# Performance work log

Hardware: AMD Instinct MI355X
Metric: run time of the kernel (lower is better)

## Reference

```python
import jax, jax.numpy as jnp
import numpy as np

NUM_HEADS = 5
TEMP = 0.3
NEG_FILL = -1e-7  # note: NOT -inf; masked entries still contribute ~exp(0) to softmax, faithful to torch code


def setup_inputs() -> dict:
    key = jax.random.key(0)
    k1, k2, k3, k4, k5 = jax.random.split(key, 5)
    B, N, F_IN, F_OUT = 8, 1024, 320, 320
    h = jax.random.normal(k1, (B, N, F_IN), dtype=jnp.float32)
    Wqk = jax.random.normal(k2, (F_IN, 2 * F_IN), dtype=jnp.float32) * (1.0 / np.sqrt(F_IN))
    bqk = jax.random.normal(k3, (2 * F_IN,), dtype=jnp.float32) * 0.01
    weight = jax.random.normal(k4, (F_IN, F_OUT), dtype=jnp.float32) * (1.0 / np.sqrt(F_OUT))
    bias = jax.random.normal(k5, (F_OUT,), dtype=jnp.float32) * 0.01
    return {"h": h, "Wqk": Wqk, "bqk": bqk, "weight": weight, "bias": bias}


def reference(h, Wqk, bqk, weight, bias):
    B, N, F = h.shape
    H = NUM_HEADS
    D = F // H
    # linear -> [b, n, 2F]; einops 'b n (h d qk)' => reshape (b, n, h, d, 2)
    qk = (h @ Wqk + bqk).reshape(B, N, H, D, 2)
    q = jnp.transpose(qk[..., 0], (0, 2, 1, 3))  # b h n d
    k = jnp.transpose(qk[..., 1], (0, 2, 1, 3))  # b h n d
    scale = D ** -0.5
    dots = jnp.einsum('bhqd,bhkd->bhqk', q, k) * scale  # b h n n
    at = dots.sum(axis=1)  # b n n  (sum over heads)
    # sort-based threshold: keep values >= descending-sorted value at index N//6
    thr = jax.lax.top_k(at, N // 6 + 1)[0][..., -1]  # b n
    adj = jnp.where(at < thr[:, :, None], jnp.asarray(NEG_FILL, at.dtype), at)
    attn = jax.nn.softmax(adj / TEMP, axis=2)  # b n n
    out_feature = jnp.einsum('bij,bjd->bid', attn, h)  # values = raw input h
    return out_feature @ weight + bias
```

## Files before the change

### kernel.cpp

```cpp
#include <hip/hip_runtime.h>
#include <hip/hip_fp16.h>


typedef __attribute__((ext_vector_type(8))) _Float16 half8;
typedef __attribute__((ext_vector_type(4))) float f32x4;

__device__ __forceinline__ void stage_tile(const __half* g, __half* lds,
                                           int nrow16, int ld, int wave, int lane) {
    const int r = lane >> 2;
    const int c = ((lane & 3) ^ ((lane >> 3) & 3)) * 8;
    for (int i = wave; i < nrow16; i += 4) {
        const __half* src = g + (long)(i * 16 + r) * ld + c;
        __builtin_amdgcn_global_load_lds(
            (const __attribute__((address_space(1))) unsigned int*)src,
            (__attribute__((address_space(3))) unsigned int*)(lds + i * 512),
            16, 0, 0);
    }
}

template <int EPI>
__device__ __forceinline__ void gemm_body(
    const __half* __restrict__ A, const __half* __restrict__ B,
    void* __restrict__ C, void* __restrict__ C2, const float* __restrict__ bias,
    int lda, int ldb, int ldc, int bx, int by, __half* smem)
{
    constexpr int BUF = 16384;
    const int tid  = threadIdx.x;
    const int lane = tid & 63;
    const int wave = tid >> 6;
    const int wm   = wave >> 1;
    const int wn   = wave & 1;

    const __half* Ab = A + (long)by * 128 * lda;
    const __half* Bb = B + (long)bx * 128 * ldb;

    f32x4 acc[4][4];
    #pragma unroll
    for (int i = 0; i < 4; ++i)
        #pragma unroll
        for (int j = 0; j < 4; ++j) acc[i][j] = (f32x4){0.f, 0.f, 0.f, 0.f};

    const int lrow = lane & 15;
    const int quad = lane >> 4;
    const int swz = (quad ^ ((lrow >> 1) & 3)) * 8;

    #pragma unroll
    for (int c = 0; c < 2; ++c) {
        stage_tile(Ab + c * 32, smem + c * 4096, 8, lda, wave, lane);
        stage_tile(Bb + c * 32, smem + 8192 + c * 4096, 8, ldb, wave, lane);
    }

    for (int it = 0; it < 5; ++it) {
        __syncthreads();
        if (it + 1 < 5) {
            __half* nb = smem + ((it + 1) & 1) * BUF;
            const int k1 = (it + 1) * 64;
            #pragma unroll
            for (int c = 0; c < 2; ++c) {
                stage_tile(Ab + k1 + c * 32, nb + c * 4096, 8, lda, wave, lane);
                stage_tile(Bb + k1 + c * 32, nb + 8192 + c * 4096, 8, ldb, wave, lane);
            }
        }
        const __half* buf = smem + (it & 1) * BUF;
        #pragma unroll
        for (int c = 0; c < 2; ++c) {
            const __half* pA = buf + c * 4096 + (wm * 64 + lrow) * 32 + swz;
            const __half* pB = buf + 8192 + c * 4096 + (wn * 64 + lrow) * 32 + swz;
            half8 ah[4], bh[4];
            #pragma unroll
            for (int mt = 0; mt < 4; ++mt) ah[mt] = *(const half8*)(pA + mt * 512);
            #pragma unroll
            for (int nt = 0; nt < 4; ++nt) bh[nt] = *(const half8*)(pB + nt * 512);
            #pragma unroll
            for (int mt = 0; mt < 4; ++mt)
                #pragma unroll
                for (int nt = 0; nt < 4; ++nt)
                    acc[mt][nt] = __builtin_amdgcn_mfma_f32_16x16x32_f16(
                        ah[mt], bh[nt], acc[mt][nt], 0, 0, 0);
        }
    }

    const int row_base = by * 128 + wm * 64;
    const int col_base = bx * 128 + wn * 64;
    #pragma unroll
    for (int mt = 0; mt < 4; ++mt)
        #pragma unroll
        for (int nt = 0; nt < 4; ++nt)
            #pragma unroll
            for (int r = 0; r < 4; ++r) {
                const int row = row_base + mt * 16 + quad * 4 + r;
                const int col = col_base + nt * 16 + lrow;
                const float v = acc[mt][nt][r];
                if (EPI == 1) {
                    const float val = v + bias[col];
                    const long idx = (long)row * 320 + (col >> 1);
                    if (col & 1) ((__half*)C2)[idx] = __float2half(val);
                    else         ((__half*)C)[idx]  = __float2half(val);
                } else {
                    ((__half*)C)[(long)row * ldc + col] = __float2half(v);
                }
            }
}

__global__ __launch_bounds__(256) void g1_combined(
    const __half* __restrict__ h16, const __half* __restrict__ wTp,
    const __half* __restrict__ WqkT, __half* __restrict__ hWT,
    __half* __restrict__ Q, __half* __restrict__ Kb,
    const float* __restrict__ bqk)
{
    __shared__ __half smem[2 * 16384];
    const int bx = blockIdx.x;
    if (bx < 192) {
        gemm_body<2>(wTp, h16, hWT, nullptr, nullptr,
                     320, 320, 8192, bx % 64, bx / 64, smem);
    } else {
        const int b = bx - 192;
        gemm_body<1>(h16, WqkT, Q, Kb, bqk,
                     320, 320, 320, b % 5, b / 5, smem);
    }
}

__global__ __launch_bounds__(256) void prep_all(
    const float* __restrict__ h, ushort4* __restrict__ h16,
    const float* __restrict__ Wqk, __half* __restrict__ WqkT,
    const float* __restrict__ weight, __half* __restrict__ wTp)
{
    const int bx = blockIdx.x;
    if (bx < 2560) {
        const int i = bx * 256 + threadIdx.x;
        const float4 v = ((const float4*)h)[i];
        ushort4 o;
        o.x = __half_as_ushort(__float2half(v.x));
        o.y = __half_as_ushort(__float2half(v.y));
        o.z = __half_as_ushort(__float2half(v.z));
        o.w = __half_as_ushort(__float2half(v.w));
        h16[i] = o;
        return;
    }
    __shared__ float t[32][33];
    const float* src;
    __half* dst;
    int ldS, ldT, c0, r0;
    if (bx < 2760) {
        const int b = bx - 2560;
        src = Wqk; dst = WqkT; ldS = 640; ldT = 320;
        c0 = (b % 20) * 32; r0 = (b / 20) * 32;
    } else {
        const int b = bx - 2760;
        src = weight; dst = wTp; ldS = 320; ldT = 320;
        c0 = (b % 10) * 32; r0 = (b / 10) * 32;
    }
    const int lx = threadIdx.x & 31, ly = threadIdx.x >> 5;
    #pragma unroll
    for (int i = 0; i < 4; ++i)
        t[ly + 8 * i][lx] = src[(long)(r0 + ly + 8 * i) * ldS + c0 + lx];
    __syncthreads();
    #pragma unroll
    for (int i = 0; i < 4; ++i)
        dst[(long)(c0 + ly + 8 * i) * ldT + r0 + lx] = __float2half(t[lx][ly + 8 * i]);
}

__global__ __launch_bounds__(512, 2) void fused_attn(
    const __half* __restrict__ Q, const __half* __restrict__ Kmat,
    const __half* __restrict__ hWT, const float* __restrict__ bias,
    float* __restrict__ out)
{
    __shared__ __half P[32768];
    __shared__ int hist[8][256];

    const int tid  = threadIdx.x;
    const int lane = tid & 63;
    const int wave = tid >> 6;
    const int lrow = lane & 15;
    const int quad = lane >> 4;

    const int b  = blockIdx.x & 7;
    const int r0 = (blockIdx.x >> 3) * 32;

    const __half* Qb = Q    + (long)(b * 1024 + r0) * 320;
    const __half* Kb = Kmat + (long)b * 327680;
    const __half* Wb = hWT  + (long)b * 1024;

    half8 qreg[10][2];
    #pragma unroll
    for (int kc = 0; kc < 10; ++kc)
        #pragma unroll
        for (int mi = 0; mi < 2; ++mi)
            qreg[kc][mi] = *(const half8*)(Qb + (long)(mi * 16 + lrow) * 320
                                           + kc * 32 + quad * 8);

    const __half* Kw = Kb + (long)(wave * 128 + lrow) * 320 + quad * 8;
    #pragma unroll
    for (int cg = 0; cg < 2; ++cg) {
        f32x4 acc[4][2];
        #pragma unroll
        for (int i = 0; i < 4; ++i)
            #pragma unroll
            for (int j = 0; j < 2; ++j) acc[i][j] = (f32x4){0.f, 0.f, 0.f, 0.f};
        #pragma unroll
        for (int kc = 0; kc < 10; ++kc) {
            half8 bh[4];
            #pragma unroll
            for (int cb = 0; cb < 4; ++cb)
                bh[cb] = *(const half8*)(Kw + (long)(cg * 64 + cb * 16) * 320
                                         + kc * 32);
            #pragma unroll
            for (int cb = 0; cb < 4; ++cb)
                #pragma unroll
                for (int mi = 0; mi < 2; ++mi)
                    acc[cb][mi] = __builtin_amdgcn_mfma_f32_16x16x32_f16(
                        qreg[kc][mi], bh[cb], acc[cb][mi], 0, 0, 0);
        }
        #pragma unroll
        for (int cb = 0; cb < 4; ++cb)
            #pragma unroll
            for (int mi = 0; mi < 2; ++mi)
                #pragma unroll
                for (int rr = 0; rr < 4; ++rr) {
                    const int row = mi * 16 + quad * 4 + rr;
                    const int col = wave * 128 + cg * 64 + cb * 16 + lrow;
                    P[((row << 10) + col) ^ ((row & 7) << 3)] =
                        __float2half(0.125f * acc[cb][mi][rr]);
                }
    }
    __syncthreads();

    for (int j = 0; j < 4; ++j) {
        const int row  = wave * 4 + j;
        const int key8 = (row & 7) << 3;
        const int base = (row << 10) + lane * 16;

        unsigned short vs[16];
        *(uint4*)&vs[0] = *(const uint4*)&P[base ^ key8];
        *(uint4*)&vs[8] = *(const uint4*)&P[(base + 8) ^ key8];

        unsigned key[16];
        #pragma unroll
        for (int i = 0; i < 16; ++i) {
            const unsigned u = vs[i];
            key[i] = (u & 0x8000u) ? ((~u) & 0xFFFFu) : (u | 0x8000u);
        }

        unsigned prefix = 0, pmask = 0;
        int kk = 171;

        #pragma unroll
        for (int pass = 0; pass < 2; ++pass) {
            const int shift = 8 - 8 * pass;
            *(int4*)&hist[wave][lane * 4] = make_int4(0, 0, 0, 0);
            __syncthreads();
            #pragma unroll
            for (int i = 0; i < 16; ++i) {
                if ((key[i] & pmask) == prefix)
                    atomicAdd(&hist[wave][(key[i] >> shift) & 255], 1);
            }
            __syncthreads();
            const int4 hh = *(const int4*)&hist[wave][lane * 4];
            const int s = hh.x + hh.y + hh.z + hh.w;
            int suf = s;
            #pragma unroll
            for (int off = 1; off < 64; off <<= 1) {
                const int o = __shfl_down(suf, off);
                if (lane + off < 64) suf += o;
            }
            const int cgt3 = suf - s;
            const int cgt2 = cgt3 + hh.w;
            const int cgt1 = cgt2 + hh.z;
            const int cgt0 = cgt1 + hh.y;
            int pick = 0x7FFFFFFF;
            if (cgt3 < kk && kk <= cgt3 + hh.w) pick = ((4 * lane + 3) << 16) | (kk - cgt3);
            if (cgt2 < kk && kk <= cgt2 + hh.z) pick = ((4 * lane + 2) << 16) | (kk - cgt2);
            if (cgt1 < kk && kk <= cgt1 + hh.y) pick = ((4 * lane + 1) << 16) | (kk - cgt1);
            if (cgt0 < kk && kk <= cgt0 + hh.x) pick = ((4 * lane + 0) << 16) | (kk - cgt0);
            #pragma unroll
            for (int off = 32; off > 0; off >>= 1) pick = min(pick, __shfl_xor(pick, off));
            const unsigned digit = (unsigned)(pick >> 16);
            kk = pick & 0xFFFF;
            prefix |= digit << shift;
            pmask  |= 0xFFu << shift;
            if (pass == 0) __syncthreads();
        }

        const unsigned short tu = (prefix & 0x8000u) ? (unsigned short)(prefix & 0x7FFFu)
                                                     : (unsigned short)((~prefix) & 0xFFFFu);
        const float thr = __half2float(__ushort_as_half(tu));

        float lg[16];
        float mx = -3.4e38f;
        #pragma unroll
        for (int i = 0; i < 16; ++i) {
            const float v = __half2float(__ushort_as_half(vs[i]));
            const float a = (v < thr) ? -1e-7f : v;
            lg[i] = a * (1.0f / 0.3f);
            mx = fmaxf(mx, lg[i]);
        }
        #pragma unroll
        for (int off = 32; off > 0; off >>= 1) mx = fmaxf(mx, __shfl_xor(mx, off));

        float e[16];
        float sum = 0.f;
        #pragma unroll
        for (int i = 0; i < 16; ++i) { e[i] = __expf(lg[i] - mx); sum += e[i]; }
        #pragma unroll
        for (int off = 32; off > 0; off >>= 1) sum += __shfl_xor(sum, off);
        const float inv = 1.0f / sum;

        unsigned short os[16];
        #pragma unroll
        for (int i = 0; i < 16; ++i) os[i] = __half_as_ushort(__float2half(e[i] * inv));
        *(uint4*)&P[base ^ key8]       = *(const uint4*)&os[0];
        *(uint4*)&P[(base + 8) ^ key8] = *(const uint4*)&os[8];
    }
    __syncthreads();

    const int q4 = wave & 3;
    const int kh = wave >> 2;

    f32x4 acc4[5][2];
    #pragma unroll
    for (int i = 0; i < 5; ++i)
        #pragma unroll
        for (int j = 0; j < 2; ++j) acc4[i][j] = (f32x4){0.f, 0.f, 0.f, 0.f};

    const __half* Wq = Wb + (long)(q4 * 80 + lrow) * 8192 + kh * 512 + quad * 8;
    #pragma unroll 4
    for (int t = 0; t < 16; ++t) {
        half8 bh[5];
        #pragma unroll
        for (int cf = 0; cf < 5; ++cf)
            bh[cf] = *(const half8*)(Wq + (long)cf * 16 * 8192 + t * 32);
        const int kk = kh * 512 + t * 32 + quad * 8;
        half8 ah[2];
        #pragma unroll
        for (int mi = 0; mi < 2; ++mi) {
            const int row = mi * 16 + lrow;
            ah[mi] = *(const half8*)&P[((row << 10) + kk) ^ ((row & 7) << 3)];
        }
        #pragma unroll
        for (int cf = 0; cf < 5; ++cf)
            #pragma unroll
            for (int mi = 0; mi < 2; ++mi)
                acc4[cf][mi] = __builtin_amdgcn_mfma_f32_16x16x32_f16(
                    ah[mi], bh[cf], acc4[cf][mi], 0, 0, 0);
    }

    __syncthreads();
    float* const red = (float*)P;
    if (kh == 1) {
        #pragma unroll
        for (int cf = 0; cf < 5; ++cf)
            #pragma unroll
            for (int mi = 0; mi < 2; ++mi)
                #pragma unroll
                for (int rr = 0; rr < 4; ++rr)
                    red[(mi * 16 + quad * 4 + rr) * 320 + q4 * 80 + cf * 16 + lrow] =
                        acc4[cf][mi][rr];
    }
    __syncthreads();
    if (kh == 0) {
        #pragma unroll
        for (int cf = 0; cf < 5; ++cf)
            #pragma unroll
            for (int mi = 0; mi < 2; ++mi)
                #pragma unroll
                for (int rr = 0; rr < 4; ++rr) {
                    const int row = mi * 16 + quad * 4 + rr;
                    const int col = q4 * 80 + cf * 16 + lrow;
                    out[(long)(b * 1024 + r0 + row) * 320 + col] =
                        acc4[cf][mi][rr] + red[row * 320 + col] + bias[col];
                }
    }
}

extern "C" void kernel_launch(void* const* d_in, const int* in_sizes, int n_in,
                              void* d_out, int out_size, void* d_ws, size_t ws_size,
                              hipStream_t stream) {
    (void)in_sizes; (void)n_in; (void)out_size; (void)ws_size;

    const float* h      = (const float*)d_in[0];
    const float* Wqk    = (const float*)d_in[1];
    const float* bqk    = (const float*)d_in[2];
    const float* weight = (const float*)d_in[3];
    const float* bias   = (const float*)d_in[4];
    float* out = (float*)d_out;

    char* p = (char*)d_ws;
    __half* h16  = (__half*)p; p += 2621440L * 2;
    __half* Q    = (__half*)p; p += 2621440L * 2;
    __half* Kb   = (__half*)p; p += 2621440L * 2;
    __half* WqkT = (__half*)p; p += 640L * 320 * 2;
    __half* wTp  = (__half*)p; p += 384L * 320 * 2;
    __half* hWT  = (__half*)p; p += 384L * 8192 * 2;

    prep_all<<<2860, 256, 0, stream>>>(h, (ushort4*)h16, Wqk, WqkT, weight, wTp);

    g1_combined<<<512, 256, 0, stream>>>(h16, wTp, WqkT, hWT, Q, Kb, bqk);

    fused_attn<<<256, 512, 0, stream>>>(Q, Kb, hWT, bias, out);
}
```

Measured before the change: 146.9 us.

## Double fused attention block to 16 waves and drop syncs in wave-private radix select

The fused attention kernel now launches 1024 threads per block instead of 512. Each wave computes 64 key columns of the score tile, loading Q per k-chunk rather than keeping all of Q in registers. Each wave handles 2 rows in the radix top-k select, and the softmax-times-V GEMM is split across row halves and key halves. The block-wide barriers around the per-wave histogram are removed, since each wave uses its own histogram row. The aim is more latency hiding and better MFMA utilization per CU with only 256 blocks, at the cost of higher register pressure under the new launch bounds and reliance on in-wave LDS ordering.

```diff
diff --git a/kernel.cpp b/kernel.cpp
--- a/kernel.cpp
+++ b/kernel.cpp
@@ -160,13 +160,13 @@
         dst[(long)(c0 + ly + 8 * i) * ldT + r0 + lx] = __float2half(t[lx][ly + 8 * i]);
 }
 
-__global__ __launch_bounds__(512, 2) void fused_attn(
+__global__ __launch_bounds__(1024, 4) void fused_attn(
     const __half* __restrict__ Q, const __half* __restrict__ Kmat,
     const __half* __restrict__ hWT, const float* __restrict__ bias,
     float* __restrict__ out)
 {
     __shared__ __half P[32768];
-    __shared__ int hist[8][256];
+    __shared__ int hist[16][256];
 
     const int tid  = threadIdx.x;
     const int lane = tid & 63;
@@ -181,52 +181,46 @@
     const __half* Kb = Kmat + (long)b * 327680;
     const __half* Wb = hWT  + (long)b * 1024;
 
-    half8 qreg[10][2];
-    #pragma unroll
-    for (int kc = 0; kc < 10; ++kc)
+    f32x4 acc[4][2];
+    #pragma unroll
+    for (int i = 0; i < 4; ++i)
+        #pragma unroll
+        for (int j = 0; j < 2; ++j) acc[i][j] = (f32x4){0.f, 0.f, 0.f, 0.f};
+
+    const __half* Qf = Qb + (long)lrow * 320 + quad * 8;
+    const __half* Kw = Kb + (long)(wave * 64 + lrow) * 320 + quad * 8;
+    #pragma unroll
+    for (int kc = 0; kc < 10; ++kc) {
+        half8 ah[2], bh[4];
         #pragma unroll
         for (int mi = 0; mi < 2; ++mi)
-            qreg[kc][mi] = *(const half8*)(Qb + (long)(mi * 16 + lrow) * 320
-                                           + kc * 32 + quad * 8);
-
-    const __half* Kw = Kb + (long)(wave * 128 + lrow) * 320 + quad * 8;
-    #pragma unroll
-    for (int cg = 0; cg < 2; ++cg) {
-        f32x4 acc[4][2];
-        #pragma unroll
-        for (int i = 0; i < 4; ++i)
-            #pragma unroll
-            for (int j = 0; j < 2; ++j) acc[i][j] = (f32x4){0.f, 0.f, 0.f, 0.f};
-        #pragma unroll
-        for (int kc = 0; kc < 10; ++kc) {
-            half8 bh[4];
-            #pragma unroll
-            for (int cb = 0; cb < 4; ++cb)
-                bh[cb] = *(const half8*)(Kw + (long)(cg * 64 + cb * 16) * 320
-                                         + kc * 32);
-            #pragma unroll
-            for (int cb = 0; cb < 4; ++cb)
-                #pragma unroll
-                for (int mi = 0; mi < 2; ++mi)
-                    acc[cb][mi] = __builtin_amdgcn_mfma_f32_16x16x32_f16(
-                        qreg[kc][mi], bh[cb], acc[cb][mi], 0, 0, 0);
-        }
+            ah[mi] = *(const half8*)(Qf + (long)mi * 16 * 320 + kc * 32);
         #pragma unroll
         for (int cb = 0; cb < 4; ++cb)
+            bh[cb] = *(const half8*)(Kw + (long)cb * 16 * 320 + kc * 32);
+        #pragma unroll
+        for (int cb = 0; cb < 4; ++cb)
             #pragma unroll
             for (int mi = 0; mi < 2; ++mi)
-                #pragma unroll
-                for (int rr = 0; rr < 4; ++rr) {
-                    const int row = mi * 16 + quad * 4 + rr;
-                    const int col = wave * 128 + cg * 64 + cb * 16 + lrow;
-                    P[((row << 10) + col) ^ ((row & 7) << 3)] =
-                        __float2half(0.125f * acc[cb][mi][rr]);
-                }
-    }
-    __syncthreads();
-
-    for (int j = 0; j < 4; ++j) {
-        const int row  = wave * 4 + j;
+                acc[cb][mi] = __builtin_amdgcn_mfma_f32_16x16x32_f16(
+                    ah[mi], bh[cb], acc[cb][mi], 0, 0, 0);
+    }
+    #pragma unroll
+    for (int cb = 0; cb < 4; ++cb)
+        #pragma unroll
+        for (int mi = 0; mi < 2; ++mi)
+            #pragma unroll
+            for (int rr = 0; rr < 4; ++rr) {
+                const int row = mi * 16 + quad * 4 + rr;
+                const int col = wave * 64 + cb * 16 + lrow;
+                P[((row << 10) + col) ^ ((row & 7) << 3)] =
+                    __float2half(0.125f * acc[cb][mi][rr]);
+            }
+    __syncthreads();
+
+    #pragma unroll
+    for (int j = 0; j < 2; ++j) {
+        const int row  = wave * 2 + j;
         const int key8 = (row & 7) << 3;
         const int base = (row << 10) + lane * 16;
 
@@ -248,13 +242,11 @@
         for (int pass = 0; pass < 2; ++pass) {
             const int shift = 8 - 8 * pass;
             *(int4*)&hist[wave][lane * 4] = make_int4(0, 0, 0, 0);
-            __syncthreads();
             #pragma unroll
             for (int i = 0; i < 16; ++i) {
                 if ((key[i] & pmask) == prefix)
                     atomicAdd(&hist[wave][(key[i] >> shift) & 255], 1);
             }
-            __syncthreads();
             const int4 hh = *(const int4*)&hist[wave][lane * 4];
             const int s = hh.x + hh.y + hh.z + hh.w;
             int suf = s;
@@ -278,7 +270,6 @@
             kk = pick & 0xFFFF;
             prefix |= digit << shift;
             pmask  |= 0xFFu << shift;
-            if (pass == 0) __syncthreads();
         }
 
         const unsigned short tu = (prefix & 0x8000u) ? (unsigned short)(prefix & 0x7FFFu)
@@ -313,35 +304,28 @@
     }
     __syncthreads();
 
-    const int q4 = wave & 3;
-    const int kh = wave >> 2;
-
-    f32x4 acc4[5][2];
-    #pragma unroll
-    for (int i = 0; i < 5; ++i)
-        #pragma unroll
-        for (int j = 0; j < 2; ++j) acc4[i][j] = (f32x4){0.f, 0.f, 0.f, 0.f};
+    const int q4  = wave & 3;
+    const int mi2 = (wave >> 2) & 1;
+    const int kh  = wave >> 3;
+
+    f32x4 acc4[5];
+    #pragma unroll
+    for (int i = 0; i < 5; ++i) acc4[i] = (f32x4){0.f, 0.f, 0.f, 0.f};
 
     const __half* Wq = Wb + (long)(q4 * 80 + lrow) * 8192 + kh * 512 + quad * 8;
-    #pragma unroll 4
+    const int rowA = mi2 * 16 + lrow;
+    #pragma unroll
     for (int t = 0; t < 16; ++t) {
         half8 bh[5];
         #pragma unroll
         for (int cf = 0; cf < 5; ++cf)
             bh[cf] = *(const half8*)(Wq + (long)cf * 16 * 8192 + t * 32);
         const int kk = kh * 512 + t * 32 + quad * 8;
-        half8 ah[2];
-        #pragma unroll
-        for (int mi = 0; mi < 2; ++mi) {
-            const int row = mi * 16 + lrow;
-            ah[mi] = *(const half8*)&P[((row << 10) + kk) ^ ((row & 7) << 3)];
-        }
+        const half8 ah = *(const half8*)&P[((rowA << 10) + kk) ^ ((rowA & 7) << 3)];
         #pragma unroll
         for (int cf = 0; cf < 5; ++cf)
-            #pragma unroll
-            for (int mi = 0; mi < 2; ++mi)
-                acc4[cf][mi] = __builtin_amdgcn_mfma_f32_16x16x32_f16(
-                    ah[mi], bh[cf], acc4[cf][mi], 0, 0, 0);
+            acc4[cf] = __builtin_amdgcn_mfma_f32_16x16x32_f16(
+                ah, bh[cf], acc4[cf], 0, 0, 0);
     }
 
     __syncthreads();
@@ -350,25 +334,21 @@
         #pragma unroll
         for (int cf = 0; cf < 5; ++cf)
             #pragma unroll
-            for (int mi = 0; mi < 2; ++mi)
-                #pragma unroll
-                for (int rr = 0; rr < 4; ++rr)
-                    red[(mi * 16 + quad * 4 + rr) * 320 + q4 * 80 + cf * 16 + lrow] =
-                        acc4[cf][mi][rr];
+            for (int rr = 0; rr < 4; ++rr)
+                red[(mi2 * 16 + quad * 4 + rr) * 320 + q4 * 80 + cf * 16 + lrow] =
+                    acc4[cf][rr];
     }
     __syncthreads();
     if (kh == 0) {
         #pragma unroll
         for (int cf = 0; cf < 5; ++cf)
             #pragma unroll
-            for (int mi = 0; mi < 2; ++mi)
-                #pragma unroll
-                for (int rr = 0; rr < 4; ++rr) {
-                    const int row = mi * 16 + quad * 4 + rr;
-                    const int col = q4 * 80 + cf * 16 + lrow;
-                    out[(long)(b * 1024 + r0 + row) * 320 + col] =
-                        acc4[cf][mi][rr] + red[row * 320 + col] + bias[col];
-                }
+            for (int rr = 0; rr < 4; ++rr) {
+                const int row = mi2 * 16 + quad * 4 + rr;
+                const int col = q4 * 80 + cf * 16 + lrow;
+                out[(long)(b * 1024 + r0 + row) * 320 + col] =
+                    acc4[cf][rr] + red[row * 320 + col] + bias[col];
+            }
     }
 }
 
@@ -396,5 +376,5 @@
 
     g1_combined<<<512, 256, 0, stream>>>(h16, wTp, WqkT, hWT, Q, Kb, bqk);
 
-    fused_attn<<<256, 512, 0, stream>>>(Q, Kb, hWT, bias, out);
-}
+    fused_attn<<<256, 1024, 0, stream>>>(Q, Kb, hWT, bias, out);
+}
```

Result: slower. 163.4 us (+11.2%).

## Stage Q, K and W tiles through LDS with per-wave double-buffered async loads

Applied to the files above, without the earlier changes.

Q is now loaded into shared memory through swizzled global_load_lds instead of being held in registers. K tiles and the hWT tiles for the second GEMM are streamed per wave into double-buffered LDS, using explicit vmcnt waits so the next tile's load overlaps the current MFMA work. The W prefetch is issued before the top-k/softmax phase so that phase can hide it, and the block-wide barriers in the per-wave histogram passes are removed because each wave has its own histogram. LDS use grows to about 152KB, which may cut occupancy, and relying on wave-local ordering without barriers is delicate.

```diff
diff --git a/kernel.cpp b/kernel.cpp
--- a/kernel.cpp
+++ b/kernel.cpp
@@ -4,12 +4,28 @@
 
 typedef __attribute__((ext_vector_type(8))) _Float16 half8;
 typedef __attribute__((ext_vector_type(4))) float f32x4;
+
+#define WAITV(N) do { asm volatile("s_waitcnt vmcnt(" #N ")" ::: "memory"); \
+                      __builtin_amdgcn_sched_barrier(0); } while (0)
 
 __device__ __forceinline__ void stage_tile(const __half* g, __half* lds,
                                            int nrow16, int ld, int wave, int lane) {
     const int r = lane >> 2;
     const int c = ((lane & 3) ^ ((lane >> 3) & 3)) * 8;
     for (int i = wave; i < nrow16; i += 4) {
+        const __half* src = g + (long)(i * 16 + r) * ld + c;
+        __builtin_amdgcn_global_load_lds(
+            (const __attribute__((address_space(1))) unsigned int*)src,
+            (__attribute__((address_space(3))) unsigned int*)(lds + i * 512),
+            16, 0, 0);
+    }
+}
+
+__device__ __forceinline__ void stage_wave(const __half* g, __half* lds,
+                                           int nrow16, int ld, int lane) {
+    const int r = lane >> 2;
+    const int c = ((lane & 3) ^ ((lane >> 3) & 3)) * 8;
+    for (int i = 0; i < nrow16; ++i) {
         const __half* src = g + (long)(i * 16 + r) * ld + c;
         __builtin_amdgcn_global_load_lds(
             (const __attribute__((address_space(1))) unsigned int*)src,
@@ -165,14 +181,20 @@
     const __half* __restrict__ hWT, const float* __restrict__ bias,
     float* __restrict__ out)
 {
-    __shared__ __half P[32768];
-    __shared__ int hist[8][256];
+    __shared__ __half smem[77824];
+    __half* const P  = smem;
+    __half* const S  = smem + 32768;
+    __half* const QL = S;
+    __half* const KB = S + 10240;
+    __half* const WB = S;
+    int (*const hist)[256] = (int(*)[256])(smem + 73728);
 
     const int tid  = threadIdx.x;
     const int lane = tid & 63;
     const int wave = tid >> 6;
     const int lrow = lane & 15;
     const int quad = lane >> 4;
+    const int swz  = (quad ^ ((lrow >> 1) & 3)) * 8;
 
     const int b  = blockIdx.x & 7;
     const int r0 = (blockIdx.x >> 3) * 32;
@@ -181,15 +203,21 @@
     const __half* Kb = Kmat + (long)b * 327680;
     const __half* Wb = hWT  + (long)b * 1024;
 
-    half8 qreg[10][2];
-    #pragma unroll
-    for (int kc = 0; kc < 10; ++kc)
-        #pragma unroll
-        for (int mi = 0; mi < 2; ++mi)
-            qreg[kc][mi] = *(const half8*)(Qb + (long)(mi * 16 + lrow) * 320
-                                           + kc * 32 + quad * 8);
-
-    const __half* Kw = Kb + (long)(wave * 128 + lrow) * 320 + quad * 8;
+    for (int i = wave; i < 20; i += 8) {
+        const int s   = i * 64 + lane;
+        const int row = s / 40;
+        const int cb  = s % 40;
+        const int gb  = cb ^ (row & 7);
+        const __half* src = Qb + (long)row * 320 + gb * 8;
+        __builtin_amdgcn_global_load_lds(
+            (const __attribute__((address_space(1))) unsigned int*)src,
+            (__attribute__((address_space(3))) unsigned int*)(QL + i * 512),
+            16, 0, 0);
+    }
+    __half* const kb0 = KB + wave * 4096;
+    stage_wave(Kb + (long)(wave * 128) * 320, kb0, 4, 320, lane);
+    __syncthreads();
+
     #pragma unroll
     for (int cg = 0; cg < 2; ++cg) {
         f32x4 acc[4][2];
@@ -197,19 +225,33 @@
         for (int i = 0; i < 4; ++i)
             #pragma unroll
             for (int j = 0; j < 2; ++j) acc[i][j] = (f32x4){0.f, 0.f, 0.f, 0.f};
-        #pragma unroll
+
         for (int kc = 0; kc < 10; ++kc) {
-            half8 bh[4];
+            const int r = cg * 10 + kc;
+            if (r + 1 < 20) {
+                const int cg1 = (r + 1) / 10, kc1 = (r + 1) % 10;
+                stage_wave(Kb + (long)(wave * 128 + cg1 * 64) * 320 + kc1 * 32,
+                           kb0 + ((r + 1) & 1) * 2048, 4, 320, lane);
+                WAITV(4);
+            } else {
+                WAITV(0);
+            }
+            const __half* kt = kb0 + (r & 1) * 2048;
+            const int gbq = kc * 4 + quad;
+            half8 ah[2], bh[4];
+            #pragma unroll
+            for (int mi = 0; mi < 2; ++mi)
+                ah[mi] = *(const half8*)&QL[(mi * 16 + lrow) * 320
+                                            + (gbq ^ (lrow & 7)) * 8];
             #pragma unroll
             for (int cb = 0; cb < 4; ++cb)
-                bh[cb] = *(const half8*)(Kw + (long)(cg * 64 + cb * 16) * 320
-                                         + kc * 32);
+                bh[cb] = *(const half8*)(kt + (cb * 16 + lrow) * 32 + swz);
             #pragma unroll
             for (int cb = 0; cb < 4; ++cb)
                 #pragma unroll
                 for (int mi = 0; mi < 2; ++mi)
                     acc[cb][mi] = __builtin_amdgcn_mfma_f32_16x16x32_f16(
-                        qreg[kc][mi], bh[cb], acc[cb][mi], 0, 0, 0);
+                        ah[mi], bh[cb], acc[cb][mi], 0, 0, 0);
         }
         #pragma unroll
         for (int cb = 0; cb < 4; ++cb)
@@ -225,6 +267,13 @@
     }
     __syncthreads();
 
+    const int q4 = wave & 3;
+    const int kh = wave >> 2;
+    __half* const wb0 = WB + wave * 5120;
+    const __half* Wbase = Wb + (long)(q4 * 80) * 8192 + kh * 512;
+    stage_wave(Wbase, wb0, 5, 8192, lane);
+
+    #pragma unroll
     for (int j = 0; j < 4; ++j) {
         const int row  = wave * 4 + j;
         const int key8 = (row & 7) << 3;
@@ -248,13 +297,11 @@
         for (int pass = 0; pass < 2; ++pass) {
             const int shift = 8 - 8 * pass;
             *(int4*)&hist[wave][lane * 4] = make_int4(0, 0, 0, 0);
-            __syncthreads();
             #pragma unroll
             for (int i = 0; i < 16; ++i) {
                 if ((key[i] & pmask) == prefix)
                     atomicAdd(&hist[wave][(key[i] >> shift) & 255], 1);
             }
-            __syncthreads();
             const int4 hh = *(const int4*)&hist[wave][lane * 4];
             const int s = hh.x + hh.y + hh.z + hh.w;
             int suf = s;
@@ -278,7 +325,6 @@
             kk = pick & 0xFFFF;
             prefix |= digit << shift;
             pmask  |= 0xFFu << shift;
-            if (pass == 0) __syncthreads();
         }
 
         const unsigned short tu = (prefix & 0x8000u) ? (unsigned short)(prefix & 0x7FFFu)
@@ -313,29 +359,31 @@
     }
     __syncthreads();
 
-    const int q4 = wave & 3;
-    const int kh = wave >> 2;
-
     f32x4 acc4[5][2];
     #pragma unroll
     for (int i = 0; i < 5; ++i)
         #pragma unroll
         for (int j = 0; j < 2; ++j) acc4[i][j] = (f32x4){0.f, 0.f, 0.f, 0.f};
 
-    const __half* Wq = Wb + (long)(q4 * 80 + lrow) * 8192 + kh * 512 + quad * 8;
-    #pragma unroll 4
     for (int t = 0; t < 16; ++t) {
-        half8 bh[5];
-        #pragma unroll
-        for (int cf = 0; cf < 5; ++cf)
-            bh[cf] = *(const half8*)(Wq + (long)cf * 16 * 8192 + t * 32);
+        if (t + 1 < 16) {
+            stage_wave(Wbase + (t + 1) * 32, wb0 + ((t + 1) & 1) * 2560,
+                       5, 8192, lane);
+            WAITV(5);
+        } else {
+            WAITV(0);
+        }
+        const __half* T = wb0 + (t & 1) * 2560;
         const int kk = kh * 512 + t * 32 + quad * 8;
-        half8 ah[2];
+        half8 ah[2], bh[5];
         #pragma unroll
         for (int mi = 0; mi < 2; ++mi) {
             const int row = mi * 16 + lrow;
             ah[mi] = *(const half8*)&P[((row << 10) + kk) ^ ((row & 7) << 3)];
         }
+        #pragma unroll
+        for (int cf = 0; cf < 5; ++cf)
+            bh[cf] = *(const half8*)(T + (cf * 16 + lrow) * 32 + swz);
         #pragma unroll
         for (int cf = 0; cf < 5; ++cf)
             #pragma unroll
```

New measurement: 126.0 us. -14.3%, faster.
